# Kernel optimization log

Hardware: AMD Instinct MI355X
Metric: run time of the kernel (lower is better)

Reference implementation:

```python
import jax, jax.numpy as jnp
import numpy as np

N = 4096          # n_nodes
M = 8192          # m_nodes (= 2*N, required by block structure)
D = 128           # in_dim == hidden_dim (conv1 is reapplied to its own output)
H = 128
NUM_ITERS = 3


def setup_inputs() -> dict:
    key = jax.random.key(0)
    ks = jax.random.split(key, 6)
    X = jax.random.normal(ks[0], (N, D), dtype=jnp.float32)
    R = jax.random.uniform(ks[1], (N, N), dtype=jnp.float32)
    A = 0.5 * (R + R.T)  # symmetric, strictly positive connectivity matrix
    # upsample MLP: Linear(n_nodes -> m_nodes - n_nodes), torch weight layout [out, in]
    W_up = jax.random.normal(ks[2], (M - N, N), dtype=jnp.float32) * 0.02
    b_up = jnp.zeros((M - N,), dtype=jnp.float32)
    # GCNConv linear weights stored [in, out]
    W1 = jax.random.normal(ks[3], (D, H), dtype=jnp.float32) * 0.05
    b1 = jnp.zeros((H,), dtype=jnp.float32)
    W2 = jax.random.normal(ks[4], (H, H), dtype=jnp.float32) * 0.05
    b2 = jnp.zeros((H,), dtype=jnp.float32)
    return dict(X=X, A=A, W_up=W_up, b_up=b_up, W1=W1, b1=b1, W2=W2, b2=b2)


def _gcn(Adj, X, W, b):
    # PyG GCNConv on a fully dense, strictly-positive weighted graph:
    # every diagonal entry is nonzero, so add_remaining_self_loops is a no-op and
    # out = D^{-1/2} A D^{-1/2} (X W) + b  exactly.
    deg = Adj.sum(axis=0)                         # [m] column degree
    dinv = jnp.where(deg > 0, jax.lax.rsqrt(deg), 0.0)
    An = Adj * dinv[:, None] * dinv[None, :]      # symmetric normalization
    return An @ (X @ W) + b


def reference(X, A, W_up, b_up, W1, b1, W2, b2):
    # new_nodes = upsample_mlp(X.T).T  -> [M-N, D]
    new_nodes = (X.T @ W_up.T + b_up).T
    Xu = jnp.concatenate([X, new_nodes], axis=0)  # [M, D]
    # block adjacency: [[A, A.T], [A, sigmoid(new @ new.T)]]
    Adj = jnp.block([[A, A.T],
                     [A, jax.nn.sigmoid(new_nodes @ new_nodes.T)]])  # [M, M]
    A_out = Adj
    for _ in range(NUM_ITERS):
        Xu = jax.nn.relu(_gcn(Adj, Xu, W1, b1))
        Adj = jax.nn.sigmoid(Xu @ Xu.T)           # mid-loop adjacency rebuild
        Xu = jax.nn.relu(_gcn(Adj, Xu, W2, b2))
        A_out = jax.nn.sigmoid(Xu @ Xu.T)
        # NOTE: edge_index for the next conv1 is NOT rebuilt from A_out in the
        # original (only after conv1), so Adj carries the mid-loop matrix.
    return A_out
```

## Files before the change

kernel.cpp:

```cpp
#include <hip/hip_runtime.h>
#include <hip/hip_bf16.h>


#define N_NODES 4096
#define M_NODES 8192
#define DIM 128
#define SLICE_ELEMS ((size_t)M_NODES * DIM)

typedef __attribute__((ext_vector_type(4))) float f32x4;
typedef __attribute__((ext_vector_type(8))) short bf16x8;

__device__ __forceinline__ unsigned short f2bf(float f) {
  union { float f; unsigned u; } v; v.f = f;
  unsigned r = v.u + 0x7fffu + ((v.u >> 16) & 1u);
  return (unsigned short)(r >> 16);
}

__device__ __forceinline__ void gld16(unsigned short* lds, const unsigned short* g) {
  __builtin_amdgcn_global_load_lds(
      (const __attribute__((address_space(1))) unsigned int*)g,
      (__attribute__((address_space(3))) unsigned int*)lds, 16, 0, 0);
}

__device__ __forceinline__ float sigmoidf_(float x) { return 1.0f / (1.0f + __expf(-x)); }


__global__ void cast_x_kernel(const float* __restrict__ X, unsigned short* __restrict__ Xu,
                              unsigned short* __restrict__ XT) {
  int idx = blockIdx.x * 256 + threadIdx.x;
  int i = idx >> 7, c = idx & 127;
  unsigned short b = f2bf(X[idx]);
  Xu[idx] = b;
  XT[(size_t)c * N_NODES + i] = b;
}

__global__ void cast_wup_kernel(const float4* __restrict__ W, unsigned short* __restrict__ Wb) {
  int idx4 = blockIdx.x * 256 + threadIdx.x;
  int r = idx4 >> 10, c = (idx4 & 1023) << 2;
  float4 v = W[idx4];
  ushort4 o;
  o.x = f2bf(v.x); o.y = f2bf(v.y); o.z = f2bf(v.z); o.w = f2bf(v.w);
  int tm = r >> 7, rr = r & 127;
  int kc = c >> 10, st = (c & 1023) >> 5, e = c & 31;
  *(ushort4*)&Wb[((size_t)tm * 4 + kc) * 131072 + (size_t)st * 4096 + rr * 32 + e] = o;
}

__global__ void cast_wt2_kernel(const float* __restrict__ W1, const float* __restrict__ W2,
                                unsigned short* __restrict__ WT1,
                                unsigned short* __restrict__ WT2) {
  int idx = blockIdx.x * 256 + threadIdx.x;
  const float* W = idx < 16384 ? W1 : W2;
  unsigned short* WT = idx < 16384 ? WT1 : WT2;
  int j = idx & 16383;
  int k = j >> 7, c = j & 127;
  WT[c * DIM + k] = f2bf(W[j]);
}

__global__ void cast_a_kernel(const float* __restrict__ A, unsigned short* __restrict__ Adj,
                              float* __restrict__ colsumA) {
  int c = blockIdx.x * 256 + threadIdx.x;
  int r0 = blockIdx.y * 128;
  int tm = r0 >> 7;
  int kc = c >> 10, st = (c & 1023) >> 5, e = c & 31;
  size_t a1 = ((size_t)(tm)      * 8 + kc)     * 131072 + (size_t)st * 4096 + e;
  size_t a2 = ((size_t)(tm)      * 8 + 4 + kc) * 131072 + (size_t)st * 4096 + e;
  size_t a3 = ((size_t)(tm + 32) * 8 + kc)     * 131072 + (size_t)st * 4096 + e;
  float s = 0.f;
  for (int r = 0; r < 128; ++r) {
    float a = A[(size_t)(r0 + r) * N_NODES + c];
    unsigned short b = f2bf(a);
    Adj[a1 + r * 32] = b; Adj[a2 + r * 32] = b; Adj[a3 + r * 32] = b;
    s += a;
  }
  atomicAdd(&colsumA[c], s);
}

__global__ void init_deg_kernel(const float* __restrict__ colsumA, float* __restrict__ deg) {
  int i = blockIdx.x * 256 + threadIdx.x;
  deg[i] = (i < N_NODES) ? 2.0f * colsumA[i] : colsumA[i - N_NODES];
}


__global__ __launch_bounds__(256, 2)
void agg_kernel(const unsigned short* __restrict__ At, long tileRowElems,
                const unsigned short* __restrict__ BT, long ldb,
                float* __restrict__ accBase, int kIters) {
  __shared__ __align__(16) unsigned short smem[24576];
  const int t = threadIdx.x, w = t >> 6, lane = t & 63;
  const int q = lane >> 4, l15 = lane & 15;
  const int sg0 = blockIdx.y * kIters;
  const size_t abase = (size_t)blockIdx.x * tileRowElems + (size_t)sg0 * 4096;
  const size_t bk = (size_t)sg0 * 32;
  const int arow = t >> 2, achk = t & 3;

  auto STAGE = [&](int s, int b) {
    unsigned short* la = smem + b * 8192;
    unsigned short* lb = la + 4096;
    gld16(&la[t * 8],        &At[abase + (size_t)s * 4096 + t * 8]);
    gld16(&la[2048 + t * 8], &At[abase + (size_t)s * 4096 + 2048 + t * 8]);
    gld16(&lb[t * 8],        &BT[(size_t)arow * ldb + bk + s * 32 + achk * 8]);
    gld16(&lb[2048 + t * 8], &BT[(size_t)(64 + arow) * ldb + bk + s * 32 + achk * 8]);
  };

  f32x4 acc[2][8];
#pragma unroll
  for (int a = 0; a < 2; ++a)
#pragma unroll
    for (int b = 0; b < 8; ++b) acc[a][b] = (f32x4)0.f;

  STAGE(0, 0);
  if (kIters > 1) STAGE(1, 1);

  for (int s = 0; s < kIters; ++s) {
    if (s + 2 < kIters) {
      STAGE(s + 2, (s + 2) % 3);
      asm volatile("s_waitcnt vmcnt(8)" ::: "memory");
    } else if (s + 1 < kIters) {
      asm volatile("s_waitcnt vmcnt(4)" ::: "memory");
    } else {
      asm volatile("s_waitcnt vmcnt(0)" ::: "memory");
    }
    __builtin_amdgcn_s_barrier();
    __builtin_amdgcn_sched_barrier(0);

    const unsigned short* la = smem + (s % 3) * 8192;
    const unsigned short* lb = la + 4096;
    bf16x8 a0 = *(const bf16x8*)&la[(w * 32 + l15) * 32 + q * 8];
    bf16x8 a1 = *(const bf16x8*)&la[(w * 32 + 16 + l15) * 32 + q * 8];
#pragma unroll
    for (int nt = 0; nt < 8; ++nt) {
      bf16x8 b = *(const bf16x8*)&lb[(nt * 16 + l15) * 32 + q * 8];
      acc[0][nt] = __builtin_amdgcn_mfma_f32_16x16x32_bf16(a0, b, acc[0][nt], 0, 0, 0);
      acc[1][nt] = __builtin_amdgcn_mfma_f32_16x16x32_bf16(a1, b, acc[1][nt], 0, 0, 0);
    }
    __builtin_amdgcn_sched_barrier(0);
    __builtin_amdgcn_s_barrier();
    __builtin_amdgcn_sched_barrier(0);
  }
  float* ct = accBase + (size_t)blockIdx.y * SLICE_ELEMS + (size_t)blockIdx.x * 16384;
#pragma unroll
  for (int mt = 0; mt < 2; ++mt)
#pragma unroll
    for (int nt = 0; nt < 8; ++nt)
      *(f32x4*)&ct[(((w * 2 + mt) * 8 + nt) * 256) + (q * 16 + l15) * 4] = acc[mt][nt];
}

__global__ void reduce_acc_kernel(const float* __restrict__ acc,
                                  unsigned short* __restrict__ dst,
                                  const float* __restrict__ bias_row,
                                  const float* __restrict__ bias_col,
                                  const float* __restrict__ deg, int mode, int nSlices) {
  int p = blockIdx.x * 256 + threadIdx.x;
  float s = 0.f;
  for (int sp = 0; sp < nSlices; ++sp) s += acc[(size_t)sp * SLICE_ELEMS + p];
  int tile = p >> 14, r = p & 16383;
  int grp = r >> 8, r2 = r & 255;
  int nt = grp & 7, wmt = grp >> 3;
  int i = r2 & 3, ql = r2 >> 2;
  int row = tile * 128 + (wmt >> 1) * 32 + (wmt & 1) * 16 + (ql >> 4) * 4 + i;
  int col = nt * 16 + (ql & 15);
  float v;
  if (mode == 0) {
    v = s + bias_row[row];
  } else {
    float d = deg[row];
    float dv = d > 0.f ? rsqrtf(d) : 0.f;
    v = fmaxf(dv * s + bias_col[col], 0.f);
  }
  dst[(size_t)row * DIM + col] = f2bf(v);
}


template <int MODE>
__global__ __launch_bounds__(256)
void rebuild_kernel(const unsigned short* __restrict__ XA,
                    const unsigned short* __restrict__ XB,
                    void* __restrict__ out, long p1 ,
                    long col0, float* __restrict__ deg) {
  __shared__ __align__(16) unsigned short smem[32768];
  __shared__ float lcol[128];
  unsigned short* lA = smem;
  unsigned short* lB = smem + 16384;
  const int t = threadIdx.x, w = t >> 6, lane = t & 63;
  const int q = lane >> 4, l15 = lane & 15;
  const int i0 = blockIdx.x * 128, j0 = blockIdx.y * 128;
  const int srow = t >> 2, schk = t & 3;
#pragma unroll
  for (int kk = 0; kk < 4; ++kk)
#pragma unroll
    for (int h = 0; h < 2; ++h) {
      gld16(&lA[kk * 4096 + h * 2048 + t * 8],
            &XA[(size_t)(i0 + h * 64 + srow) * DIM + kk * 32 + schk * 8]);
      gld16(&lB[kk * 4096 + h * 2048 + t * 8],
            &XB[(size_t)(j0 + h * 64 + srow) * DIM + kk * 32 + schk * 8]);
    }
  if (MODE == 0 && t < 128) lcol[t] = 0.f;
  __syncthreads();

  f32x4 acc[2][8];
#pragma unroll
  for (int a = 0; a < 2; ++a)
#pragma unroll
    for (int b = 0; b < 8; ++b) acc[a][b] = (f32x4)0.f;

#pragma unroll
  for (int kk = 0; kk < 4; ++kk) {
    bf16x8 a0 = *(const bf16x8*)&lA[kk * 4096 + (w * 32 + l15) * 32 + q * 8];
    bf16x8 a1 = *(const bf16x8*)&lA[kk * 4096 + (w * 32 + 16 + l15) * 32 + q * 8];
#pragma unroll
    for (int nt = 0; nt < 8; ++nt) {
      bf16x8 b = *(const bf16x8*)&lB[kk * 4096 + (nt * 16 + l15) * 32 + q * 8];
      acc[0][nt] = __builtin_amdgcn_mfma_f32_16x16x32_bf16(a0, b, acc[0][nt], 0, 0, 0);
      acc[1][nt] = __builtin_amdgcn_mfma_f32_16x16x32_bf16(a1, b, acc[1][nt], 0, 0, 0);
    }
  }
  __syncthreads();

  if (MODE == 0) {
    unsigned short* lC = smem;
#pragma unroll
    for (int mt = 0; mt < 2; ++mt)
#pragma unroll
      for (int nt = 0; nt < 8; ++nt) {
        float cs = 0.f;
#pragma unroll
        for (int i = 0; i < 4; ++i) {
          float sv = sigmoidf_(acc[mt][nt][i]);
          cs += sv;
          lC[(w * 32 + mt * 16 + q * 4 + i) * 136 + nt * 16 + l15] = f2bf(sv);
        }
        cs += __shfl_xor(cs, 16);
        cs += __shfl_xor(cs, 32);
        if (lane < 16) atomicAdd(&lcol[nt * 16 + lane], cs);
      }
    __syncthreads();
    unsigned short* og = (unsigned short*)out;
    const long rowbase = p1 + i0, colbase = col0 + j0;
    const size_t tb = ((size_t)(rowbase >> 7) * 8 + (colbase >> 10)) * 131072;
    const int stb = (int)((colbase & 1023) >> 5);
#pragma unroll
    for (int cc = 0; cc < 8; ++cc) {
      int ch = t + cc * 256;
      int row = ch >> 4, c16 = ch & 15;
      *(bf16x8*)&og[tb + (size_t)(stb + (c16 >> 2)) * 4096 + row * 32 + (c16 & 3) * 8] =
          *(const bf16x8*)&lC[row * 136 + c16 * 8];
    }
    if (t < 128) atomicAdd(&deg[colbase + t], lcol[t]);
  } else {
    float* og = (float*)out;
    float* lCf = (float*)smem;
#pragma unroll
    for (int h2 = 0; h2 < 2; ++h2) {
      __syncthreads();
      if ((w >> 1) == h2) {
#pragma unroll
        for (int mt = 0; mt < 2; ++mt)
#pragma unroll
          for (int nt = 0; nt < 8; ++nt)
#pragma unroll
            for (int i = 0; i < 4; ++i)
              lCf[((w & 1) * 32 + mt * 16 + q * 4 + i) * 128 + nt * 16 + l15] =
                  sigmoidf_(acc[mt][nt][i]);
      }
      __syncthreads();
#pragma unroll
      for (int j = 0; j < 8; ++j) {
        int ch = t + j * 256;
        int r64 = ch >> 5, c4 = (ch & 31) * 4;
        *(f32x4*)&og[(size_t)(i0 + h2 * 64 + r64) * p1 + j0 + c4] =
            *(const f32x4*)&lCf[r64 * 128 + c4];
      }
    }
  }
}


__global__ __launch_bounds__(256)
void yz_kernel(const unsigned short* __restrict__ Xu, const unsigned short* __restrict__ WT,
               const float* __restrict__ deg, unsigned short* __restrict__ ZT, int ldz) {
  __shared__ __align__(16) unsigned short smem[32768];
  unsigned short* lA = smem;
  unsigned short* lB = smem + 16384;
  const int t = threadIdx.x, w = t >> 6, lane = t & 63;
  const int q = lane >> 4, l15 = lane & 15;
  const int r0 = blockIdx.x * 128;
  const int srow = t >> 2, schk = t & 3;
#pragma unroll
  for (int kk = 0; kk < 4; ++kk)
#pragma unroll
    for (int h = 0; h < 2; ++h) {
      gld16(&lA[kk * 4096 + h * 2048 + t * 8],
            &Xu[(size_t)(r0 + h * 64 + srow) * DIM + kk * 32 + schk * 8]);
      gld16(&lB[kk * 4096 + h * 2048 + t * 8],
            &WT[(size_t)(h * 64 + srow) * DIM + kk * 32 + schk * 8]);
    }
  __syncthreads();

  f32x4 acc[2][8];
#pragma unroll
  for (int a = 0; a < 2; ++a)
#pragma unroll
    for (int b = 0; b < 8; ++b) acc[a][b] = (f32x4)0.f;

#pragma unroll
  for (int kk = 0; kk < 4; ++kk) {
    bf16x8 a0 = *(const bf16x8*)&lA[kk * 4096 + (w * 32 + l15) * 32 + q * 8];
    bf16x8 a1 = *(const bf16x8*)&lA[kk * 4096 + (w * 32 + 16 + l15) * 32 + q * 8];
#pragma unroll
    for (int nt = 0; nt < 8; ++nt) {
      bf16x8 b = *(const bf16x8*)&lB[kk * 4096 + (nt * 16 + l15) * 32 + q * 8];
      acc[0][nt] = __builtin_amdgcn_mfma_f32_16x16x32_bf16(a0, b, acc[0][nt], 0, 0, 0);
      acc[1][nt] = __builtin_amdgcn_mfma_f32_16x16x32_bf16(a1, b, acc[1][nt], 0, 0, 0);
    }
  }
  __syncthreads();
  unsigned short* lT = smem;
#pragma unroll
  for (int mt = 0; mt < 2; ++mt)
#pragma unroll
    for (int i = 0; i < 4; ++i) {
      int r = w * 32 + mt * 16 + q * 4 + i;
      float d = deg[r0 + r];
      float dv = d > 0.f ? rsqrtf(d) : 0.f;
#pragma unroll
      for (int nt = 0; nt < 8; ++nt)
        lT[(nt * 16 + l15) * 136 + r] = f2bf(dv * acc[mt][nt][i]);
    }
  __syncthreads();
#pragma unroll
  for (int cc = 0; cc < 8; ++cc) {
    int ch = t + cc * 256;
    int c = ch >> 4, c16 = ch & 15;
    *(bf16x8*)&ZT[(size_t)c * ldz + r0 + c16 * 8] = *(const bf16x8*)&lT[c * 136 + c16 * 8];
  }
}


extern "C" void kernel_launch(void* const* d_in, const int* in_sizes, int n_in,
                              void* d_out, int out_size, void* d_ws, size_t ws_size,
                              hipStream_t stream) {
  (void)in_sizes; (void)n_in; (void)out_size;
  const float* X   = (const float*)d_in[0];
  const float* A   = (const float*)d_in[1];
  const float* Wup = (const float*)d_in[2];
  const float* bup = (const float*)d_in[3];
  const float* W1  = (const float*)d_in[4];
  const float* b1  = (const float*)d_in[5];
  const float* W2  = (const float*)d_in[6];
  const float* b2  = (const float*)d_in[7];

  const size_t ADJ_BYTES = (size_t)M_NODES * M_NODES * 2;
  char* ws = (char*)d_ws;
  size_t off = 0;
  auto alloc = [&](size_t bytes) {
    char* p = ws + off;
    off += (bytes + 255) & ~(size_t)255;
    return p;
  };
  float*          accb    = (float*)alloc(16 * SLICE_ELEMS * 4);
  unsigned short* Xu      = (unsigned short*)alloc((size_t)M_NODES * DIM * 2);
  unsigned short* ZT      = (unsigned short*)alloc((size_t)DIM * M_NODES * 2);
  unsigned short* XT      = (unsigned short*)alloc((size_t)DIM * N_NODES * 2);
  unsigned short* W1T     = (unsigned short*)alloc(DIM * DIM * 2);
  unsigned short* W2T     = (unsigned short*)alloc(DIM * DIM * 2);
  float*          colsumA = (float*)alloc(N_NODES * 4);
  float*          deg     = (float*)alloc(M_NODES * 4);

  unsigned short* Adj;
  if (ws_size >= off + ADJ_BYTES) Adj = (unsigned short*)(ws + off);
  else                            Adj = (unsigned short*)d_out;
  unsigned short* Wupb = Adj;

  unsigned short* XuNew = Xu + (size_t)N_NODES * DIM;

  hipMemsetAsync(colsumA, 0, N_NODES * 4, stream);
  cast_x_kernel<<<N_NODES * DIM / 256, 256, 0, stream>>>(X, Xu, XT);
  cast_wup_kernel<<<((size_t)N_NODES * N_NODES / 4) / 256, 256, 0, stream>>>(
      (const float4*)Wup, Wupb);
  cast_wt2_kernel<<<128, 256, 0, stream>>>(W1, W2, W1T, W2T);

  agg_kernel<<<dim3(N_NODES / 128, 16), 256, 0, stream>>>(
      Wupb, 4L * 131072, XT, N_NODES, accb, 8);
  reduce_acc_kernel<<<N_NODES * DIM / 256, 256, 0, stream>>>(
      accb, XuNew, bup, nullptr, nullptr, 0, 16);

  cast_a_kernel<<<dim3(N_NODES / 256, N_NODES / 128), 256, 0, stream>>>(A, Adj, colsumA);
  init_deg_kernel<<<M_NODES / 256, 256, 0, stream>>>(colsumA, deg);
  rebuild_kernel<0><<<dim3(N_NODES / 128, N_NODES / 128), 256, 0, stream>>>(
      XuNew, XuNew, Adj, N_NODES, N_NODES, deg);

  for (int it = 0; it < 3; ++it) {
    yz_kernel<<<M_NODES / 128, 256, 0, stream>>>(Xu, W1T, deg, ZT, M_NODES);
    agg_kernel<<<dim3(M_NODES / 128, 8), 256, 0, stream>>>(
        Adj, 8L * 131072, ZT, M_NODES, accb, 32);
    reduce_acc_kernel<<<M_NODES * DIM / 256, 256, 0, stream>>>(
        accb, Xu, nullptr, b1, deg, 1, 8);
    hipMemsetAsync(deg, 0, M_NODES * 4, stream);
    rebuild_kernel<0><<<dim3(M_NODES / 128, M_NODES / 128), 256, 0, stream>>>(
        Xu, Xu, Adj, 0, 0, deg);
    yz_kernel<<<M_NODES / 128, 256, 0, stream>>>(Xu, W2T, deg, ZT, M_NODES);
    agg_kernel<<<dim3(M_NODES / 128, 8), 256, 0, stream>>>(
        Adj, 8L * 131072, ZT, M_NODES, accb, 32);
    reduce_acc_kernel<<<M_NODES * DIM / 256, 256, 0, stream>>>(
        accb, Xu, nullptr, b2, deg, 1, 8);
    if (it == 2)
      rebuild_kernel<1><<<dim3(M_NODES / 128, M_NODES / 128), 256, 0, stream>>>(
          Xu, Xu, d_out, M_NODES, 0, nullptr);
  }
}
```

Before: 974.7 us.

## Fuse sigmoid adjacency recompute into aggregation instead of materializing Adj

Adds a fused_conv kernel that recomputes sigmoid(X_j·X_i) tiles on the fly from node features and multiplies them straight into Z, so the 8192x8192 bf16 adjacency is never written or re-read after the first iteration. The rebuild kernel gets a mode that only accumulates column degrees, and a row-major reduce kernel replaces the tiled reduce. This trades roughly 128 MB of adjacency traffic per conv for a second set of MFMAs and extra exp work per tile, with ping-pong feature buffers kept so the previous iteration's adjacency can be regenerated.

```diff
diff --git a/kernel.cpp b/kernel.cpp
--- a/kernel.cpp
+++ b/kernel.cpp
@@ -170,6 +170,19 @@
   dst[(size_t)row * DIM + col] = f2bf(v);
 }
 
+__global__ void reduce_rm_kernel(const float* __restrict__ acc,
+                                 unsigned short* __restrict__ dst,
+                                 const float* __restrict__ bias_col,
+                                 const float* __restrict__ deg, int nSlices) {
+  int p = blockIdx.x * 256 + threadIdx.x;
+  float s = 0.f;
+  for (int sp = 0; sp < nSlices; ++sp) s += acc[(size_t)sp * SLICE_ELEMS + p];
+  int row = p >> 7, col = p & 127;
+  float d = deg[row];
+  float dv = d > 0.f ? rsqrtf(d) : 0.f;
+  dst[p] = f2bf(fmaxf(dv * s + bias_col[col], 0.f));
+}
+
 
 template <int MODE>
 __global__ __launch_bounds__(256)
@@ -194,7 +207,7 @@
       gld16(&lB[kk * 4096 + h * 2048 + t * 8],
             &XB[(size_t)(j0 + h * 64 + srow) * DIM + kk * 32 + schk * 8]);
     }
-  if (MODE == 0 && t < 128) lcol[t] = 0.f;
+  if (MODE != 1 && t < 128) lcol[t] = 0.f;
   __syncthreads();
 
   f32x4 acc[2][8];
@@ -216,7 +229,7 @@
   }
   __syncthreads();
 
-  if (MODE == 0) {
+  if (MODE == 0 || MODE == 2) {
     unsigned short* lC = smem;
 #pragma unroll
     for (int mt = 0; mt < 2; ++mt)
@@ -227,25 +240,28 @@
         for (int i = 0; i < 4; ++i) {
           float sv = sigmoidf_(acc[mt][nt][i]);
           cs += sv;
-          lC[(w * 32 + mt * 16 + q * 4 + i) * 136 + nt * 16 + l15] = f2bf(sv);
+          if (MODE == 0)
+            lC[(w * 32 + mt * 16 + q * 4 + i) * 136 + nt * 16 + l15] = f2bf(sv);
         }
         cs += __shfl_xor(cs, 16);
         cs += __shfl_xor(cs, 32);
         if (lane < 16) atomicAdd(&lcol[nt * 16 + lane], cs);
       }
     __syncthreads();
-    unsigned short* og = (unsigned short*)out;
-    const long rowbase = p1 + i0, colbase = col0 + j0;
-    const size_t tb = ((size_t)(rowbase >> 7) * 8 + (colbase >> 10)) * 131072;
-    const int stb = (int)((colbase & 1023) >> 5);
-#pragma unroll
-    for (int cc = 0; cc < 8; ++cc) {
-      int ch = t + cc * 256;
-      int row = ch >> 4, c16 = ch & 15;
-      *(bf16x8*)&og[tb + (size_t)(stb + (c16 >> 2)) * 4096 + row * 32 + (c16 & 3) * 8] =
-          *(const bf16x8*)&lC[row * 136 + c16 * 8];
-    }
-    if (t < 128) atomicAdd(&deg[colbase + t], lcol[t]);
+    if (MODE == 0) {
+      unsigned short* og = (unsigned short*)out;
+      const long rowbase = p1 + i0, colbase = col0 + j0;
+      const size_t tb = ((size_t)(rowbase >> 7) * 8 + (colbase >> 10)) * 131072;
+      const int stb = (int)((colbase & 1023) >> 5);
+#pragma unroll
+      for (int cc = 0; cc < 8; ++cc) {
+        int ch = t + cc * 256;
+        int row = ch >> 4, c16 = ch & 15;
+        *(bf16x8*)&og[tb + (size_t)(stb + (c16 >> 2)) * 4096 + row * 32 + (c16 & 3) * 8] =
+            *(const bf16x8*)&lC[row * 136 + c16 * 8];
+      }
+    }
+    if (t < 128) atomicAdd(&deg[col0 + j0 + t], lcol[t]);
   } else {
     float* og = (float*)out;
     float* lCf = (float*)smem;
@@ -272,6 +288,78 @@
       }
     }
   }
+}
+
+
+__global__ __launch_bounds__(256, 2)
+void fused_conv(const unsigned short* __restrict__ XS,
+                const unsigned short* __restrict__ ZT,
+                float* __restrict__ accBase, int jtPerSplit) {
+  __shared__ __align__(16) unsigned short lX[16384];
+  __shared__ __align__(16) unsigned short lZ[16384];
+  __shared__ __align__(16) unsigned short lP[8192];
+  const int t = threadIdx.x, w = t >> 6, lane = t & 63;
+  const int q = lane >> 4, l15 = lane & 15;
+  const int i0 = blockIdx.x * 64;
+  const int jt0 = blockIdx.y * jtPerSplit;
+  const int z = l15 & 7;
+
+  bf16x8 xi[4];
+#pragma unroll
+  for (int kk = 0; kk < 4; ++kk)
+    xi[kk] = *(const bf16x8*)&XS[(size_t)(i0 + w * 16 + l15) * DIM + kk * 32 + q * 8];
+
+  f32x4 po[8];
+#pragma unroll
+  for (int b = 0; b < 8; ++b) po[b] = (f32x4)0.f;
+
+  for (int s = 0; s < jtPerSplit; ++s) {
+    const size_t jn0 = (size_t)(jt0 + s) * 128;
+    __syncthreads();
+#pragma unroll
+    for (int h = 0; h < 8; ++h) {
+      int g = h * 256 + t;
+      int row = g >> 4, c = g & 15;
+      int cx = (c ^ (row & 7)) * 8;
+      gld16(&lX[g * 8], &XS[(jn0 + row) * DIM + cx]);
+      gld16(&lZ[g * 8], &ZT[(size_t)row * M_NODES + jn0 + cx]);
+    }
+    __syncthreads();
+
+    f32x4 sa[8];
+#pragma unroll
+    for (int b = 0; b < 8; ++b) sa[b] = (f32x4)0.f;
+#pragma unroll
+    for (int kk = 0; kk < 4; ++kk)
+#pragma unroll
+      for (int nt = 0; nt < 8; ++nt) {
+        bf16x8 b = *(const bf16x8*)&lX[(nt * 16 + l15) * 128 + ((kk * 4 + q) ^ z) * 8];
+        sa[nt] = __builtin_amdgcn_mfma_f32_16x16x32_bf16(xi[kk], b, sa[nt], 0, 0, 0);
+      }
+#pragma unroll
+    for (int nt = 0; nt < 8; ++nt)
+#pragma unroll
+      for (int i = 0; i < 4; ++i) {
+        int col = nt * 16 + l15;
+        lP[(nt >> 1) * 2048 + (w * 16 + q * 4 + i) * 32 + (col & 31)] =
+            f2bf(sigmoidf_(sa[nt][i]));
+      }
+#pragma unroll
+    for (int kk = 0; kk < 4; ++kk) {
+      bf16x8 a = *(const bf16x8*)&lP[kk * 2048 + (w * 16 + l15) * 32 + q * 8];
+#pragma unroll
+      for (int nt = 0; nt < 8; ++nt) {
+        bf16x8 b = *(const bf16x8*)&lZ[(nt * 16 + l15) * 128 + ((kk * 4 + q) ^ z) * 8];
+        po[nt] = __builtin_amdgcn_mfma_f32_16x16x32_bf16(a, b, po[nt], 0, 0, 0);
+      }
+    }
+  }
+  float* dst = accBase + (size_t)blockIdx.y * SLICE_ELEMS;
+#pragma unroll
+  for (int nt = 0; nt < 8; ++nt)
+#pragma unroll
+    for (int i = 0; i < 4; ++i)
+      dst[(size_t)(i0 + w * 16 + q * 4 + i) * DIM + nt * 16 + l15] = po[nt][i];
 }
 
 
@@ -359,6 +447,8 @@
   };
   float*          accb    = (float*)alloc(16 * SLICE_ELEMS * 4);
   unsigned short* Xu      = (unsigned short*)alloc((size_t)M_NODES * DIM * 2);
+  unsigned short* Sa      = (unsigned short*)alloc((size_t)M_NODES * DIM * 2);
+  unsigned short* Sb      = (unsigned short*)alloc((size_t)M_NODES * DIM * 2);
   unsigned short* ZT      = (unsigned short*)alloc((size_t)DIM * M_NODES * 2);
   unsigned short* XT      = (unsigned short*)alloc((size_t)DIM * N_NODES * 2);
   unsigned short* W1T     = (unsigned short*)alloc(DIM * DIM * 2);
@@ -389,20 +479,26 @@
   rebuild_kernel<0><<<dim3(N_NODES / 128, N_NODES / 128), 256, 0, stream>>>(
       XuNew, XuNew, Adj, N_NODES, N_NODES, deg);
 
+  unsigned short* Sgen = Sa;
   for (int it = 0; it < 3; ++it) {
     yz_kernel<<<M_NODES / 128, 256, 0, stream>>>(Xu, W1T, deg, ZT, M_NODES);
-    agg_kernel<<<dim3(M_NODES / 128, 8), 256, 0, stream>>>(
-        Adj, 8L * 131072, ZT, M_NODES, accb, 32);
-    reduce_acc_kernel<<<M_NODES * DIM / 256, 256, 0, stream>>>(
-        accb, Xu, nullptr, b1, deg, 1, 8);
+    if (it == 0) {
+      agg_kernel<<<dim3(M_NODES / 128, 8), 256, 0, stream>>>(
+          Adj, 8L * 131072, ZT, M_NODES, accb, 32);
+      reduce_acc_kernel<<<M_NODES * DIM / 256, 256, 0, stream>>>(
+          accb, Sgen, nullptr, b1, deg, 1, 8);
+    } else {
+      unsigned short* Sprev = (it == 1) ? Sa : Sb;
+      Sgen = (it == 1) ? Sb : Sa;
+      fused_conv<<<dim3(M_NODES / 64, 4), 256, 0, stream>>>(Sprev, ZT, accb, 16);
+      reduce_rm_kernel<<<M_NODES * DIM / 256, 256, 0, stream>>>(accb, Sgen, b1, deg, 4);
+    }
     hipMemsetAsync(deg, 0, M_NODES * 4, stream);
-    rebuild_kernel<0><<<dim3(M_NODES / 128, M_NODES / 128), 256, 0, stream>>>(
-        Xu, Xu, Adj, 0, 0, deg);
-    yz_kernel<<<M_NODES / 128, 256, 0, stream>>>(Xu, W2T, deg, ZT, M_NODES);
-    agg_kernel<<<dim3(M_NODES / 128, 8), 256, 0, stream>>>(
-        Adj, 8L * 131072, ZT, M_NODES, accb, 32);
-    reduce_acc_kernel<<<M_NODES * DIM / 256, 256, 0, stream>>>(
-        accb, Xu, nullptr, b2, deg, 1, 8);
+    rebuild_kernel<2><<<dim3(M_NODES / 128, M_NODES / 128), 256, 0, stream>>>(
+        Sgen, Sgen, nullptr, 0, 0, deg);
+    yz_kernel<<<M_NODES / 128, 256, 0, stream>>>(Sgen, W2T, deg, ZT, M_NODES);
+    fused_conv<<<dim3(M_NODES / 64, 4), 256, 0, stream>>>(Sgen, ZT, accb, 16);
+    reduce_rm_kernel<<<M_NODES * DIM / 256, 256, 0, stream>>>(accb, Xu, b2, deg, 4);
     if (it == 2)
       rebuild_kernel<1><<<dim3(M_NODES / 128, M_NODES / 128), 256, 0, stream>>>(
           Xu, Xu, d_out, M_NODES, 0, nullptr);
```

Measured after the change: 1.177 ms. 20.8% more time.

## Exploit symmetry of sigmoid(X X^T) by computing only upper-triangular tiles

Applied to the files above, without the earlier changes.

The rebuild kernel now launches only upper-triangular 128x128 tiles (including the diagonal) and, for off-diagonal tiles, writes the transposed tile as well, computing row sums for the mirrored degree contribution. This roughly halves the MFMA and sigmoid work for the symmetric adjacency and final output. Memset calls are folded into existing kernels, and the degree buffers are double-buffered to avoid separate clears. The cost is extra LDS for a transposed staging buffer, extra atomics, and a serial loop to decode the triangular block index.

```diff
diff --git a/kernel.cpp b/kernel.cpp
--- a/kernel.cpp
+++ b/kernel.cpp
@@ -26,8 +26,10 @@
 
 
 __global__ void cast_x_kernel(const float* __restrict__ X, unsigned short* __restrict__ Xu,
-                              unsigned short* __restrict__ XT) {
+                              unsigned short* __restrict__ XT,
+                              float* __restrict__ colsumA) {
   int idx = blockIdx.x * 256 + threadIdx.x;
+  if (idx < N_NODES) colsumA[idx] = 0.f;
   int i = idx >> 7, c = idx & 127;
   unsigned short b = f2bf(X[idx]);
   Xu[idx] = b;
@@ -176,14 +178,21 @@
 void rebuild_kernel(const unsigned short* __restrict__ XA,
                     const unsigned short* __restrict__ XB,
                     void* __restrict__ out, long p1 ,
-                    long col0, float* __restrict__ deg) {
-  __shared__ __align__(16) unsigned short smem[32768];
+                    long col0, float* __restrict__ deg, int nB) {
+  __shared__ __align__(16) unsigned short smem[34816];
   __shared__ float lcol[128];
+  __shared__ float lrow[128];
   unsigned short* lA = smem;
   unsigned short* lB = smem + 16384;
   const int t = threadIdx.x, w = t >> 6, lane = t & 63;
   const int q = lane >> 4, l15 = lane & 15;
-  const int i0 = blockIdx.x * 128, j0 = blockIdx.y * 128;
+
+  int rem = blockIdx.x, bi = 0;
+  while (rem >= nB - bi) { rem -= nB - bi; ++bi; }
+  const int bj = bi + rem;
+  const int i0 = bi * 128, j0 = bj * 128;
+  const bool offdiag = (bi != bj);
+
   const int srow = t >> 2, schk = t & 3;
 #pragma unroll
   for (int kk = 0; kk < 4; ++kk)
@@ -194,7 +203,7 @@
       gld16(&lB[kk * 4096 + h * 2048 + t * 8],
             &XB[(size_t)(j0 + h * 64 + srow) * DIM + kk * 32 + schk * 8]);
     }
-  if (MODE == 0 && t < 128) lcol[t] = 0.f;
+  if (MODE == 0 && t < 128) { lcol[t] = 0.f; lrow[t] = 0.f; }
   __syncthreads();
 
   f32x4 acc[2][8];
@@ -217,7 +226,9 @@
   __syncthreads();
 
   if (MODE == 0) {
-    unsigned short* lC = smem;
+    unsigned short* lC  = smem;
+    unsigned short* lCt = smem + 17408;
+    float rs[2][4] = {{0.f, 0.f, 0.f, 0.f}, {0.f, 0.f, 0.f, 0.f}};
 #pragma unroll
     for (int mt = 0; mt < 2; ++mt)
 #pragma unroll
@@ -227,29 +238,64 @@
         for (int i = 0; i < 4; ++i) {
           float sv = sigmoidf_(acc[mt][nt][i]);
           cs += sv;
-          lC[(w * 32 + mt * 16 + q * 4 + i) * 136 + nt * 16 + l15] = f2bf(sv);
+          unsigned short hb = f2bf(sv);
+          int row = w * 32 + mt * 16 + q * 4 + i, colL = nt * 16 + l15;
+          lC[row * 136 + colL] = hb;
+          if (offdiag) { lCt[colL * 136 + row] = hb; rs[mt][i] += sv; }
         }
         cs += __shfl_xor(cs, 16);
         cs += __shfl_xor(cs, 32);
         if (lane < 16) atomicAdd(&lcol[nt * 16 + lane], cs);
       }
+    if (offdiag) {
+#pragma unroll
+      for (int mt = 0; mt < 2; ++mt)
+#pragma unroll
+        for (int i = 0; i < 4; ++i) {
+          float v = rs[mt][i];
+          v += __shfl_xor(v, 1); v += __shfl_xor(v, 2);
+          v += __shfl_xor(v, 4); v += __shfl_xor(v, 8);
+          if (l15 == 0) atomicAdd(&lrow[w * 32 + mt * 16 + q * 4 + i], v);
+        }
+    }
     __syncthreads();
     unsigned short* og = (unsigned short*)out;
-    const long rowbase = p1 + i0, colbase = col0 + j0;
-    const size_t tb = ((size_t)(rowbase >> 7) * 8 + (colbase >> 10)) * 131072;
-    const int stb = (int)((colbase & 1023) >> 5);
-#pragma unroll
-    for (int cc = 0; cc < 8; ++cc) {
-      int ch = t + cc * 256;
-      int row = ch >> 4, c16 = ch & 15;
-      *(bf16x8*)&og[tb + (size_t)(stb + (c16 >> 2)) * 4096 + row * 32 + (c16 & 3) * 8] =
-          *(const bf16x8*)&lC[row * 136 + c16 * 8];
-    }
-    if (t < 128) atomicAdd(&deg[colbase + t], lcol[t]);
+    {
+      const long rowbase = p1 + i0, colbase = col0 + j0;
+      const size_t tb = ((size_t)(rowbase >> 7) * 8 + (colbase >> 10)) * 131072;
+      const int stb = (int)((colbase & 1023) >> 5);
+#pragma unroll
+      for (int cc = 0; cc < 8; ++cc) {
+        int ch = t + cc * 256;
+        int row = ch >> 4, c16 = ch & 15;
+        *(bf16x8*)&og[tb + (size_t)(stb + (c16 >> 2)) * 4096 + row * 32 + (c16 & 3) * 8] =
+            *(const bf16x8*)&lC[row * 136 + c16 * 8];
+      }
+    }
+    if (offdiag) {
+      const long rowbase = p1 + j0, colbase = col0 + i0;
+      const size_t tb = ((size_t)(rowbase >> 7) * 8 + (colbase >> 10)) * 131072;
+      const int stb = (int)((colbase & 1023) >> 5);
+#pragma unroll
+      for (int cc = 0; cc < 8; ++cc) {
+        int ch = t + cc * 256;
+        int row = ch >> 4, c16 = ch & 15;
+        *(bf16x8*)&og[tb + (size_t)(stb + (c16 >> 2)) * 4096 + row * 32 + (c16 & 3) * 8] =
+            *(const bf16x8*)&lCt[row * 136 + c16 * 8];
+      }
+    }
+    if (t < 128) atomicAdd(&deg[col0 + j0 + t], lcol[t]);
+    if (offdiag && t < 128) atomicAdd(&deg[col0 + i0 + t], lrow[t]);
   } else {
     float* og = (float*)out;
     float* lCf = (float*)smem;
 #pragma unroll
+    for (int mt = 0; mt < 2; ++mt)
+#pragma unroll
+      for (int nt = 0; nt < 8; ++nt)
+#pragma unroll
+        for (int i = 0; i < 4; ++i) acc[mt][nt][i] = sigmoidf_(acc[mt][nt][i]);
+#pragma unroll
     for (int h2 = 0; h2 < 2; ++h2) {
       __syncthreads();
       if ((w >> 1) == h2) {
@@ -259,8 +305,8 @@
           for (int nt = 0; nt < 8; ++nt)
 #pragma unroll
             for (int i = 0; i < 4; ++i)
-              lCf[((w & 1) * 32 + mt * 16 + q * 4 + i) * 128 + nt * 16 + l15] =
-                  sigmoidf_(acc[mt][nt][i]);
+              lCf[((w & 1) * 32 + mt * 16 + q * 4 + i) * 132 + nt * 16 + l15] =
+                  acc[mt][nt][i];
       }
       __syncthreads();
 #pragma unroll
@@ -268,7 +314,31 @@
         int ch = t + j * 256;
         int r64 = ch >> 5, c4 = (ch & 31) * 4;
         *(f32x4*)&og[(size_t)(i0 + h2 * 64 + r64) * p1 + j0 + c4] =
-            *(const f32x4*)&lCf[r64 * 128 + c4];
+            *(const f32x4*)&lCf[r64 * 132 + c4];
+      }
+    }
+    if (offdiag) {
+#pragma unroll
+      for (int h2 = 0; h2 < 2; ++h2) {
+        __syncthreads();
+#pragma unroll
+        for (int mt = 0; mt < 2; ++mt)
+#pragma unroll
+          for (int nt = 0; nt < 8; ++nt)
+            if ((nt >> 2) == h2) {
+#pragma unroll
+              for (int i = 0; i < 4; ++i)
+                lCf[((nt & 3) * 16 + l15) * 132 + (w * 32 + mt * 16 + q * 4 + i)] =
+                    acc[mt][nt][i];
+            }
+        __syncthreads();
+#pragma unroll
+        for (int j = 0; j < 8; ++j) {
+          int ch = t + j * 256;
+          int r64 = ch >> 5, c4 = (ch & 31) * 4;
+          *(f32x4*)&og[(size_t)(j0 + h2 * 64 + r64) * p1 + i0 + c4] =
+              *(const f32x4*)&lCf[r64 * 132 + c4];
+        }
       }
     }
   }
@@ -277,13 +347,18 @@
 
 __global__ __launch_bounds__(256)
 void yz_kernel(const unsigned short* __restrict__ Xu, const unsigned short* __restrict__ WT,
-               const float* __restrict__ deg, unsigned short* __restrict__ ZT, int ldz) {
+               const float* __restrict__ deg, unsigned short* __restrict__ ZT, int ldz,
+               float* __restrict__ zbuf) {
   __shared__ __align__(16) unsigned short smem[32768];
   unsigned short* lA = smem;
   unsigned short* lB = smem + 16384;
   const int t = threadIdx.x, w = t >> 6, lane = t & 63;
   const int q = lane >> 4, l15 = lane & 15;
   const int r0 = blockIdx.x * 128;
+  if (zbuf) {
+    int gid = blockIdx.x * 256 + t;
+    if (gid < M_NODES) zbuf[gid] = 0.f;
+  }
   const int srow = t >> 2, schk = t & 3;
 #pragma unroll
   for (int kk = 0; kk < 4; ++kk)
@@ -364,7 +439,8 @@
   unsigned short* W1T     = (unsigned short*)alloc(DIM * DIM * 2);
   unsigned short* W2T     = (unsigned short*)alloc(DIM * DIM * 2);
   float*          colsumA = (float*)alloc(N_NODES * 4);
-  float*          deg     = (float*)alloc(M_NODES * 4);
+  float*          degA    = (float*)alloc(M_NODES * 4);
+  float*          degB    = (float*)alloc(M_NODES * 4);
 
   unsigned short* Adj;
   if (ws_size >= off + ADJ_BYTES) Adj = (unsigned short*)(ws + off);
@@ -373,8 +449,7 @@
 
   unsigned short* XuNew = Xu + (size_t)N_NODES * DIM;
 
-  hipMemsetAsync(colsumA, 0, N_NODES * 4, stream);
-  cast_x_kernel<<<N_NODES * DIM / 256, 256, 0, stream>>>(X, Xu, XT);
+  cast_x_kernel<<<N_NODES * DIM / 256, 256, 0, stream>>>(X, Xu, XT, colsumA);
   cast_wup_kernel<<<((size_t)N_NODES * N_NODES / 4) / 256, 256, 0, stream>>>(
       (const float4*)Wup, Wupb);
   cast_wt2_kernel<<<128, 256, 0, stream>>>(W1, W2, W1T, W2T);
@@ -385,26 +460,28 @@
       accb, XuNew, bup, nullptr, nullptr, 0, 16);
 
   cast_a_kernel<<<dim3(N_NODES / 256, N_NODES / 128), 256, 0, stream>>>(A, Adj, colsumA);
-  init_deg_kernel<<<M_NODES / 256, 256, 0, stream>>>(colsumA, deg);
-  rebuild_kernel<0><<<dim3(N_NODES / 128, N_NODES / 128), 256, 0, stream>>>(
-      XuNew, XuNew, Adj, N_NODES, N_NODES, deg);
-
+  init_deg_kernel<<<M_NODES / 256, 256, 0, stream>>>(colsumA, degA);
+  rebuild_kernel<0><<<32 * 33 / 2, 256, 0, stream>>>(
+      XuNew, XuNew, Adj, N_NODES, N_NODES, degA, 32);
+
+  float* degCur = degA;
+  float* degMid = degB;
   for (int it = 0; it < 3; ++it) {
-    yz_kernel<<<M_NODES / 128, 256, 0, stream>>>(Xu, W1T, deg, ZT, M_NODES);
+    yz_kernel<<<M_NODES / 128, 256, 0, stream>>>(Xu, W1T, degCur, ZT, M_NODES, degMid);
     agg_kernel<<<dim3(M_NODES / 128, 8), 256, 0, stream>>>(
         Adj, 8L * 131072, ZT, M_NODES, accb, 32);
     reduce_acc_kernel<<<M_NODES * DIM / 256, 256, 0, stream>>>(
-        accb, Xu, nullptr, b1, deg, 1, 8);
-    hipMemsetAsync(deg, 0, M_NODES * 4, stream);
-    rebuild_kernel<0><<<dim3(M_NODES / 128, M_NODES / 128), 256, 0, stream>>>(
-        Xu, Xu, Adj, 0, 0, deg);
-    yz_kernel<<<M_NODES / 128, 256, 0, stream>>>(Xu, W2T, deg, ZT, M_NODES);
+        accb, Xu, nullptr, b1, degCur, 1, 8);
+    rebuild_kernel<0><<<64 * 65 / 2, 256, 0, stream>>>(
+        Xu, Xu, Adj, 0, 0, degMid, 64);
+    yz_kernel<<<M_NODES / 128, 256, 0, stream>>>(Xu, W2T, degMid, ZT, M_NODES, nullptr);
     agg_kernel<<<dim3(M_NODES / 128, 8), 256, 0, stream>>>(
         Adj, 8L * 131072, ZT, M_NODES, accb, 32);
     reduce_acc_kernel<<<M_NODES * DIM / 256, 256, 0, stream>>>(
-        accb, Xu, nullptr, b2, deg, 1, 8);
+        accb, Xu, nullptr, b2, degMid, 1, 8);
     if (it == 2)
-      rebuild_kernel<1><<<dim3(M_NODES / 128, M_NODES / 128), 256, 0, stream>>>(
-          Xu, Xu, d_out, M_NODES, 0, nullptr);
-  }
-}
+      rebuild_kernel<1><<<64 * 65 / 2, 256, 0, stream>>>(
+          Xu, Xu, d_out, M_NODES, 0, nullptr, 64);
+    float* tmp = degCur; degCur = degMid; degMid = tmp;
+  }
+}
```

Result: faster. 933.6 us (-4.2%).
